# Kernel optimization log

Measured on AMD Instinct MI355X. Metric: run time of the kernel, lower is better.

Reference implementation:

```python
import jax, jax.numpy as jnp
import numpy as np

FIR = (1.0, 3.0, 3.0, 1.0)
FACTOR = 2
GAIN = 1.0


def _fir_kernel_2d():
    # _setup_kernel: 1D -> outer product, normalize, then scale by gain*factor^2
    k = np.asarray(FIR, dtype=np.float32)
    k = np.outer(k, k)
    k /= k.sum()
    return k * (GAIN * FACTOR ** 2)  # [4, 4]


def setup_inputs() -> dict:
    key = jax.random.key(0)
    kx, kw = jax.random.split(key)
    x = jax.random.normal(kx, (4, 256, 64, 64), dtype=jnp.float32)
    # DDPM variance-scaling init ~ U(-sqrt(3*var), sqrt(3*var)); plain scaled normal is fine for a numeric baseline
    w = jax.random.normal(kw, (256, 256, 3, 3), dtype=jnp.float32) * 0.02  # [outC, inC, 3, 3]
    return {"x": x, "w": w}


def reference(x, w):
    # Fused upsample(+FIR) conv: torch does conv_transpose2d(x, flip(w).permute(in,out), stride=2)
    # which is exactly a correlation of the stride-2 zero-dilated input with the ORIGINAL OIHW weight.
    N, C, H, W = x.shape
    outC, inC, kh, kw_ = w.shape
    h = jax.lax.conv_general_dilated(
        x, w,
        window_strides=(1, 1),
        padding=((kh - 1, kh - 1), (kw_ - 1, kw_ - 1)),
        lhs_dilation=(FACTOR, FACTOR),
        dimension_numbers=("NCHW", "OIHW", "NCHW"),
    )  # [N, outC, 2H+1, 2W+1]

    k = jnp.asarray(_fir_kernel_2d())  # [4,4]
    p = k.shape[0] - FACTOR - (kw_ - 1)          # = 0
    pad0 = (p + 1) // 2 + FACTOR - 1             # = 1
    pad1 = p // 2 + 1                            # = 1
    # upfirdn2d with up=1, down=1, pad=(pad0,pad1): pad then TRUE convolution (flipped kernel),
    # applied depthwise per channel.
    kflip = k[::-1, ::-1]
    kern = jnp.tile(kflip[None, None, :, :], (outC, 1, 1, 1))  # [outC, 1, 4, 4]
    out = jax.lax.conv_general_dilated(
        h, kern,
        window_strides=(1, 1),
        padding=((pad0, pad1), (pad0, pad1)),
        dimension_numbers=("NCHW", "OIHW", "NCHW"),
        feature_group_count=outC,
    )  # [N, outC, 2H, 2W]
    return out
```

## Files before the change

### kernel.cpp

```cpp
#include <hip/hip_runtime.h>
#include <hip/hip_bf16.h>


typedef short short2v __attribute__((ext_vector_type(2)));
typedef short bf16x8 __attribute__((ext_vector_type(8)));
typedef short short4v __attribute__((ext_vector_type(4)));
typedef float f32x2v __attribute__((ext_vector_type(2)));
typedef float f32x16 __attribute__((ext_vector_type(16)));
typedef float f32x4v __attribute__((ext_vector_type(4)));

static __device__ __forceinline__ short f2bf(float f) {
  __hip_bfloat16 h = __float2bfloat16(f);
  union { __hip_bfloat16 h; short s; } u; u.h = h;
  return u.s;
}
static __device__ __forceinline__ float bf2f(short s) {
  union { unsigned u; float f; } v; v.u = ((unsigned)(unsigned short)s) << 16;
  return v.f;
}

#define AS_SZ 18432
#define XS_BASE 36864
#define XS_SZ 8640
#define XS_STRIDE 48

__global__ __launch_bounds__(512, 2)
void fir_up_v17(const float* __restrict__ x, const float* __restrict__ w,
                float* __restrict__ out) {
  __shared__ __align__(16) char smem[54144];

  const int bid = blockIdx.x;
  const int wg = (bid & 7) * 64 + (bid >> 3);
  const int octile = wg >> 7;
  const int n = (wg >> 5) & 3;
  const int sp = wg & 31;
  const int atile = sp >> 2;
  const int btile = sp & 3;
  const int A0 = atile * 8, B0 = btile * 16;

  const int tid = threadIdx.x;
  const int wid = tid >> 6;
  const int lane = tid & 63;
  const int l31 = lane & 31, q = lane >> 5;

  const int COLSt[4]  = {17, 18, 17, 18};
  const int CELLSt[4] = {153, 162, 170, 180};
  const int NKt[4]    = {4, 2, 2, 1};
  const int KQt[4][4] = {{0,2,6,8},{1,7,7,7},{3,5,5,5},{4,4,4,4}};
  const int DYt[4][4] = {{0,0,1,1},{0,1,1,1},{0,0,0,0},{0,0,0,0}};
  const int DXt[4][4] = {{0,1,0,1},{0,0,0,0},{0,1,1,1},{0,0,0,0}};
  const int SEG0P[8]   = {0,0,0,1,1,2,2,3};
  const int SEG0FGB[8] = {0,2,4,0,3,0,3,0};
  const int SEG0NFG[8] = {2,2,1,3,3,3,3,4};

  const int p0w = SEG0P[wid];
  const int nk0 = NKt[p0w];
  const int nfg0 = SEG0NFG[wid];
  int aoff0[4];
#pragma unroll
  for (int s = 0; s < 4; ++s)
    aoff0[s] = KQt[p0w][s] * 2048 + l31 * 32 + q * 16;
  int boff0[4][4], valid0[4], hbase0[4];
#pragma unroll
  for (int fg = 0; fg < 4; ++fg) {
    const int cellraw = (SEG0FGB[wid] + fg) * 32 + l31;
    const int valid = cellraw < CELLSt[p0w];
    const int cell = valid ? cellraw : 0;
    const int cols = COLSt[p0w];
    const int r = cell / cols;
    const int c = cell - r * cols;
    valid0[fg] = valid;
    hbase0[fg] = p0w * 6400 + r * 20 + c;
#pragma unroll
    for (int s = 0; s < 4; ++s) {
      const int bc = (r + DYt[p0w][s]) * 18 + (c + DXt[p0w][s]);
      boff0[fg][s] = bc * XS_STRIDE + q * 16;
    }
  }
  const int aoff1 = 4 * 2048 + l31 * 32 + q * 16;
  int boff1[2], valid1[2], hbase1[2];
#pragma unroll
  for (int j = 0; j < 2; ++j) {
    const int cellraw = (4 + j) * 32 + l31;
    const int valid = cellraw < 180;
    const int cell = valid ? cellraw : 0;
    const int r = cell / 18;
    const int c = cell - r * 18;
    valid1[j] = valid;
    hbase1[j] = 3 * 6400 + r * 20 + c;
    boff1[j] = cell * XS_STRIDE + q * 16;
  }

  f32x16 acc[4][2];
#pragma unroll
  for (int fg = 0; fg < 4; ++fg)
#pragma unroll
    for (int mf = 0; mf < 2; ++mf)
#pragma unroll
      for (int e = 0; e < 16; ++e) acc[fg][mf][e] = 0.f;

  const int ocA = tid >> 3, icp = tid & 7;
  const float* wA = w + (size_t)(octile * 64 + ocA) * 2304 + icp * 18;
  int uic_[2], urow_[2], uf4g_[2], ugh_[2], ugw0_[2], uwb0_[2];
  bool uact_[2], urowok_[2], ual_[2], uint_[2];
#pragma unroll
  for (int t = 0; t < 2; ++t) {
    const int u = tid + t * 512;
    uact_[t] = u < 960;
    const int uu = uact_[t] ? u : 0;
    uic_[t] = uu / 60;
    const int rem = uu - uic_[t] * 60;
    urow_[t] = rem / 6;
    uf4g_[t] = rem - urow_[t] * 6;
    ugh_[t] = A0 - 1 + urow_[t];
    urowok_[t] = (ugh_[t] >= 0) & (ugh_[t] < 64);
    ugw0_[t] = B0 - 4 + 4 * uf4g_[t];
    ual_[t] = (ugw0_[t] >= 0) & (ugw0_[t] <= 60);
    uint_[t] = (uf4g_[t] >= 1) & (uf4g_[t] <= 4);
    uwb0_[t] = (urow_[t] * 18 + (4 * uf4g_[t] - 3)) * XS_STRIDE + uic_[t] * 2;
  }

  {
    char* xsw = smem + XS_BASE;
#pragma unroll
    for (int t = 0; t < 2; ++t) {
      if (uact_[t]) {
        float v[4] = {0.f, 0.f, 0.f, 0.f};
        if (urowok_[t]) {
          const float* base = x + (((size_t)(n * 256 + uic_[t])) * 64 + ugh_[t]) * 64;
          if (ual_[t]) {
            const f32x4v fv = *(const f32x4v*)(base + ugw0_[t]);
#pragma unroll
            for (int e = 0; e < 4; ++e) v[e] = fv[e];
          } else {
#pragma unroll
            for (int e = 0; e < 4; ++e) {
              const int gw = ugw0_[t] + e;
              v[e] = (gw >= 0 && gw < 64) ? base[gw] : 0.f;
            }
          }
        }
        if (uint_[t]) {
#pragma unroll
          for (int e = 0; e < 4; ++e)
            *(short*)(xsw + uwb0_[t] + e * XS_STRIDE) = f2bf(v[e]);
        } else {
#pragma unroll
          for (int e = 0; e < 4; ++e) {
            const int ww = 4 * uf4g_[t] + e - 3;
            if (ww >= 0 && ww < 18)
              *(short*)(xsw + (urow_[t] * 18 + ww) * XS_STRIDE + uic_[t] * 2) = f2bf(v[e]);
          }
        }
      }
    }
    float f18[18];
#pragma unroll
    for (int j = 0; j < 9; ++j)
      *(f32x2v*)&f18[2 * j] = *(const f32x2v*)(wA + 2 * j);
#pragma unroll
    for (int kq = 0; kq < 9; ++kq) {
      short2v pk;
      pk[0] = f2bf(f18[kq]);
      pk[1] = f2bf(f18[kq + 9]);
      *(short2v*)(smem + kq * 2048 + ocA * 32 + icp * 4) = pk;
    }
  }
  __syncthreads();

  for (int cc = 0; cc < 16; ++cc) {
    char* Asr = smem + (cc & 1) * AS_SZ;
    char* xsr = smem + XS_BASE + (cc & 1) * XS_SZ;
    char* Asw = smem + ((cc + 1) & 1) * AS_SZ;
    char* xsw = smem + XS_BASE + ((cc + 1) & 1) * XS_SZ;
    const bool have = cc < 15;

    float xv[2][4];
#pragma unroll
    for (int t = 0; t < 2; ++t) {
#pragma unroll
      for (int e = 0; e < 4; ++e) xv[t][e] = 0.f;
      if (have && uact_[t] && urowok_[t]) {
        const float* base =
            x + (((size_t)(n * 256 + (cc + 1) * 16 + uic_[t])) * 64 + ugh_[t]) * 64;
        if (ual_[t]) {
          const f32x4v fv = *(const f32x4v*)(base + ugw0_[t]);
#pragma unroll
          for (int e = 0; e < 4; ++e) xv[t][e] = fv[e];
        } else {
#pragma unroll
          for (int e = 0; e < 4; ++e) {
            const int gw = ugw0_[t] + e;
            xv[t][e] = (gw >= 0 && gw < 64) ? base[gw] : 0.f;
          }
        }
      }
    }

    __builtin_amdgcn_s_setprio(1);
#pragma unroll
    for (int s = 0; s < 4; ++s) {
      if (s < nk0) {
        const bf16x8 Aa = *(const bf16x8*)(Asr + aoff0[s]);
        const bf16x8 Ab = *(const bf16x8*)(Asr + aoff0[s] + 1024);
#pragma unroll
        for (int fg = 0; fg < 4; ++fg) {
          if (fg < nfg0) {
            const bf16x8 B = *(const bf16x8*)(xsr + boff0[fg][s]);
            acc[fg][0] = __builtin_amdgcn_mfma_f32_32x32x16_bf16(Aa, B, acc[fg][0], 0, 0, 0);
            acc[fg][1] = __builtin_amdgcn_mfma_f32_32x32x16_bf16(Ab, B, acc[fg][1], 0, 0, 0);
          }
        }
      }
    }
    if (wid == 2) {
      const bf16x8 Aa = *(const bf16x8*)(Asr + aoff1);
      const bf16x8 Ab = *(const bf16x8*)(Asr + aoff1 + 1024);
#pragma unroll
      for (int j = 0; j < 2; ++j) {
        const bf16x8 B = *(const bf16x8*)(xsr + boff1[j]);
        acc[1 + j][0] = __builtin_amdgcn_mfma_f32_32x32x16_bf16(Aa, B, acc[1 + j][0], 0, 0, 0);
        acc[1 + j][1] = __builtin_amdgcn_mfma_f32_32x32x16_bf16(Ab, B, acc[1 + j][1], 0, 0, 0);
      }
    }
    __builtin_amdgcn_s_setprio(0);

    if (have) {
#pragma unroll
      for (int t = 0; t < 2; ++t) {
        if (uact_[t]) {
          if (uint_[t]) {
#pragma unroll
            for (int e = 0; e < 4; ++e)
              *(short*)(xsw + uwb0_[t] + e * XS_STRIDE) = f2bf(xv[t][e]);
          } else {
#pragma unroll
            for (int e = 0; e < 4; ++e) {
              const int ww = 4 * uf4g_[t] + e - 3;
              if (ww >= 0 && ww < 18)
                *(short*)(xsw + (urow_[t] * 18 + ww) * XS_STRIDE + uic_[t] * 2) = f2bf(xv[t][e]);
            }
          }
        }
      }
      float f18[18];
      const float* wp = wA + (cc + 1) * 144;
#pragma unroll
      for (int j = 0; j < 9; ++j)
        *(f32x2v*)&f18[2 * j] = *(const f32x2v*)(wp + 2 * j);
#pragma unroll
      for (int kq = 0; kq < 9; ++kq) {
        short2v pk;
        pk[0] = f2bf(f18[kq]);
        pk[1] = f2bf(f18[kq + 9]);
        *(short2v*)(Asw + kq * 2048 + ocA * 32 + icp * 4) = pk;
      }
    }
    __syncthreads();
  }

  short* hl = (short*)smem;
  const float kf4[4] = {0.25f, 0.75f, 0.75f, 0.25f};
#pragma unroll
  for (int mf = 0; mf < 2; ++mf) {
    if (mf) __syncthreads();
#pragma unroll
    for (int fg = 0; fg < 4; ++fg) {
      if (fg < nfg0 && valid0[fg]) {
#pragma unroll
        for (int e = 0; e < 16; ++e) {
          const int ocl = (e & 3) + 8 * (e >> 2) + 4 * q;
          hl[hbase0[fg] + ocl * 200] = f2bf(acc[fg][mf][e]);
        }
      }
    }
    if (wid == 2) {
#pragma unroll
      for (int j = 0; j < 2; ++j) {
        if (valid1[j]) {
#pragma unroll
          for (int e = 0; e < 16; ++e) {
            const int ocl = (e & 3) + 8 * (e >> 2) + 4 * q;
            hl[hbase1[j] + ocl * 200] = f2bf(acc[1 + j][mf][e]);
          }
        }
      }
    }
    __syncthreads();
#pragma unroll
    for (int k = 0; k < 4; ++k) {
      const int v = tid + k * 512;
      const int g = v & 3;
      const int Yl = (v >> 2) & 15;
      const int ocl = v >> 6;
      float o[8];
#pragma unroll
      for (int xx = 0; xx < 8; ++xx) o[xx] = 0.f;
#pragma unroll
      for (int du = 0; du < 4; ++du) {
        const int ttp = Yl - 1 + du;
        const int py = ttp & 1;
        const int r = py ? ((Yl + du) >> 1) : (ttp >> 1);
        const int baseE = (py * 2) * 6400 + ocl * 200 + r * 20 + 4 * g;
        const int baseO = (py * 2 + 1) * 6400 + ocl * 200 + r * 20 + 4 * g;
        const short4v e0 = *(const short4v*)(hl + baseE);
        const short4v e1 = *(const short4v*)(hl + baseE + 4);
        const short4v o0 = *(const short4v*)(hl + baseO);
        const short4v o1 = *(const short4v*)(hl + baseO + 4);
        float E[8], O[8];
#pragma unroll
        for (int i = 0; i < 4; ++i) {
          E[i] = bf2f(e0[i]); E[i + 4] = bf2f(e1[i]);
          O[i] = bf2f(o0[i]); O[i + 4] = bf2f(o1[i]);
        }
        float rx[8];
        rx[0] = 0.25f*O[0] + 0.75f*E[0] + 0.75f*O[1] + 0.25f*E[1];
        rx[1] = 0.25f*E[0] + 0.75f*O[1] + 0.75f*E[1] + 0.25f*O[2];
        rx[2] = 0.25f*O[1] + 0.75f*E[1] + 0.75f*O[2] + 0.25f*E[2];
        rx[3] = 0.25f*E[1] + 0.75f*O[2] + 0.75f*E[2] + 0.25f*O[3];
        rx[4] = 0.25f*O[2] + 0.75f*E[2] + 0.75f*O[3] + 0.25f*E[3];
        rx[5] = 0.25f*E[2] + 0.75f*O[3] + 0.75f*E[3] + 0.25f*O[4];
        rx[6] = 0.25f*O[3] + 0.75f*E[3] + 0.75f*O[4] + 0.25f*E[4];
        rx[7] = 0.25f*E[3] + 0.75f*O[4] + 0.75f*E[4] + 0.25f*O[5];
        const float ky = kf4[du];
#pragma unroll
        for (int xx = 0; xx < 8; ++xx) o[xx] += ky * rx[xx];
      }
      const int oc = octile * 64 + mf * 32 + ocl;
      const int Y = atile * 16 + Yl;
      const int X0 = btile * 32 + g * 8;
      float* op = out + (((size_t)(n * 256 + oc)) * 128 + Y) * 128 + X0;
      f32x4v v0, v1;
      v0[0] = o[0]; v0[1] = o[1]; v0[2] = o[2]; v0[3] = o[3];
      v1[0] = o[4]; v1[1] = o[5]; v1[2] = o[6]; v1[3] = o[7];
      *(f32x4v*)op = v0;
      *(f32x4v*)(op + 4) = v1;
    }
  }
}

extern "C" void kernel_launch(void* const* d_in, const int* in_sizes, int n_in,
                              void* d_out, int out_size, void* d_ws, size_t ws_size,
                              hipStream_t stream) {
  (void)in_sizes; (void)n_in; (void)out_size; (void)d_ws; (void)ws_size;
  const float* x = (const float*)d_in[0];
  const float* w = (const float*)d_in[1];
  float* out = (float*)d_out;
  hipLaunchKernelGGL(fir_up_v17, dim3(512), dim3(512), 0, stream, x, w, out);
}
```

Baseline: 85.31 us.

## Double input-channel chunk per stage and rebalance phase-3 MFMA work across waves

Each pipeline stage now stages 32 input channels instead of 16, so the main loop runs 8 iterations with half as many barriers. Each stage issues two K=16 MFMA halves per A/B fragment. The next stage's weight loads are moved ahead of the MFMA block so their latency overlaps compute. One phase-3 fragment group moves from wave 7 to wave 0 to even out MFMA counts. The cost is that LDS per block grows to about 118 KB, which likely leaves room for only one 512-thread block per CU despite the launch bound of 2, and the larger staging also raises register pressure.

```diff
diff --git a/kernel.cpp b/kernel.cpp
--- a/kernel.cpp
+++ b/kernel.cpp
@@ -2,10 +2,9 @@
 #include <hip/hip_bf16.h>
 
 
-typedef short short2v __attribute__((ext_vector_type(2)));
+typedef short bf16x4v __attribute__((ext_vector_type(4)));
 typedef short bf16x8 __attribute__((ext_vector_type(8)));
 typedef short short4v __attribute__((ext_vector_type(4)));
-typedef float f32x2v __attribute__((ext_vector_type(2)));
 typedef float f32x16 __attribute__((ext_vector_type(16)));
 typedef float f32x4v __attribute__((ext_vector_type(4)));
 
@@ -19,15 +18,17 @@
   return v.f;
 }
 
-#define AS_SZ 18432
-#define XS_BASE 36864
-#define XS_SZ 8640
-#define XS_STRIDE 48
+#define AS_SZ 46080
+#define KQ_PLANE 5120
+#define AB_OFF 2560
+#define XS_BASE 92160
+#define XS_SZ 14400
+#define XS_STRIDE 80
 
 __global__ __launch_bounds__(512, 2)
-void fir_up_v17(const float* __restrict__ x, const float* __restrict__ w,
+void fir_up_v18(const float* __restrict__ x, const float* __restrict__ w,
                 float* __restrict__ out) {
-  __shared__ __align__(16) char smem[54144];
+  __shared__ __align__(16) char smem[120960];
 
   const int bid = blockIdx.x;
   const int wg = (bid & 7) * 64 + (bid >> 3);
@@ -51,7 +52,7 @@
   const int DXt[4][4] = {{0,1,0,1},{0,0,0,0},{0,1,1,1},{0,0,0,0}};
   const int SEG0P[8]   = {0,0,0,1,1,2,2,3};
   const int SEG0FGB[8] = {0,2,4,0,3,0,3,0};
-  const int SEG0NFG[8] = {2,2,1,3,3,3,3,4};
+  const int SEG0NFG[8] = {2,2,1,3,3,3,3,3};
 
   const int p0w = SEG0P[wid];
   const int nk0 = NKt[p0w];
@@ -59,10 +60,10 @@
   int aoff0[4];
 #pragma unroll
   for (int s = 0; s < 4; ++s)
-    aoff0[s] = KQt[p0w][s] * 2048 + l31 * 32 + q * 16;
-  int boff0[4][4], valid0[4], hbase0[4];
-#pragma unroll
-  for (int fg = 0; fg < 4; ++fg) {
+    aoff0[s] = KQt[p0w][s] * KQ_PLANE + l31 * 80 + q * 16;
+  int boff0[3][4], valid0[3], hbase0[3];
+#pragma unroll
+  for (int fg = 0; fg < 3; ++fg) {
     const int cellraw = (SEG0FGB[wid] + fg) * 32 + l31;
     const int valid = cellraw < CELLSt[p0w];
     const int cell = valid ? cellraw : 0;
@@ -77,36 +78,43 @@
       boff0[fg][s] = bc * XS_STRIDE + q * 16;
     }
   }
-  const int aoff1 = 4 * 2048 + l31 * 32 + q * 16;
+  const int aoff1 = 4 * KQ_PLANE + l31 * 80 + q * 16;
+  int boffW0, hbaseW0;
+  {
+    const int cell = 96 + l31;
+    const int r = cell / 18, c = cell - r * 18;
+    hbaseW0 = 3 * 6400 + r * 20 + c;
+    boffW0 = cell * XS_STRIDE + q * 16;
+  }
   int boff1[2], valid1[2], hbase1[2];
 #pragma unroll
   for (int j = 0; j < 2; ++j) {
     const int cellraw = (4 + j) * 32 + l31;
     const int valid = cellraw < 180;
     const int cell = valid ? cellraw : 0;
-    const int r = cell / 18;
-    const int c = cell - r * 18;
+    const int r = cell / 18, c = cell - r * 18;
     valid1[j] = valid;
     hbase1[j] = 3 * 6400 + r * 20 + c;
     boff1[j] = cell * XS_STRIDE + q * 16;
   }
 
-  f32x16 acc[4][2];
-#pragma unroll
-  for (int fg = 0; fg < 4; ++fg)
+  f32x16 acc[3][2];
+#pragma unroll
+  for (int fg = 0; fg < 3; ++fg)
 #pragma unroll
     for (int mf = 0; mf < 2; ++mf)
 #pragma unroll
       for (int e = 0; e < 16; ++e) acc[fg][mf][e] = 0.f;
 
-  const int ocA = tid >> 3, icp = tid & 7;
-  const float* wA = w + (size_t)(octile * 64 + ocA) * 2304 + icp * 18;
-  int uic_[2], urow_[2], uf4g_[2], ugh_[2], ugw0_[2], uwb0_[2];
-  bool uact_[2], urowok_[2], ual_[2], uint_[2];
-#pragma unroll
-  for (int t = 0; t < 2; ++t) {
+  const int ocA = tid >> 3, icq = tid & 7;
+  const float* wA = w + (size_t)(octile * 64 + ocA) * 2304 + icq * 36;
+  const int awb = ocA * 80 + icq * 8;
+  int uic_[4], urow_[4], uf4g_[4], ugh_[4], ugw0_[4], uwb0_[4];
+  bool uact_[4], urowok_[4], ual_[4], uint_[4];
+#pragma unroll
+  for (int t = 0; t < 4; ++t) {
     const int u = tid + t * 512;
-    uact_[t] = u < 960;
+    uact_[t] = u < 1920;
     const int uu = uact_[t] ? u : 0;
     uic_[t] = uu / 60;
     const int rem = uu - uic_[t] * 60;
@@ -123,7 +131,7 @@
   {
     char* xsw = smem + XS_BASE;
 #pragma unroll
-    for (int t = 0; t < 2; ++t) {
+    for (int t = 0; t < 4; ++t) {
       if (uact_[t]) {
         float v[4] = {0.f, 0.f, 0.f, 0.f};
         if (urowok_[t]) {
@@ -154,35 +162,35 @@
         }
       }
     }
-    float f18[18];
+    float f36[36];
 #pragma unroll
     for (int j = 0; j < 9; ++j)
-      *(f32x2v*)&f18[2 * j] = *(const f32x2v*)(wA + 2 * j);
+      *(f32x4v*)&f36[4 * j] = *(const f32x4v*)(wA + 4 * j);
 #pragma unroll
     for (int kq = 0; kq < 9; ++kq) {
-      short2v pk;
-      pk[0] = f2bf(f18[kq]);
-      pk[1] = f2bf(f18[kq + 9]);
-      *(short2v*)(smem + kq * 2048 + ocA * 32 + icp * 4) = pk;
+      bf16x4v pk;
+#pragma unroll
+      for (int v = 0; v < 4; ++v) pk[v] = f2bf(f36[v * 9 + kq]);
+      *(bf16x4v*)(smem + kq * KQ_PLANE + awb) = pk;
     }
   }
   __syncthreads();
 
-  for (int cc = 0; cc < 16; ++cc) {
+  for (int cc = 0; cc < 8; ++cc) {
     char* Asr = smem + (cc & 1) * AS_SZ;
     char* xsr = smem + XS_BASE + (cc & 1) * XS_SZ;
     char* Asw = smem + ((cc + 1) & 1) * AS_SZ;
     char* xsw = smem + XS_BASE + ((cc + 1) & 1) * XS_SZ;
-    const bool have = cc < 15;
-
-    float xv[2][4];
-#pragma unroll
-    for (int t = 0; t < 2; ++t) {
+    const bool have = cc < 7;
+
+    float xv[4][4];
+#pragma unroll
+    for (int t = 0; t < 4; ++t) {
 #pragma unroll
       for (int e = 0; e < 4; ++e) xv[t][e] = 0.f;
       if (have && uact_[t] && urowok_[t]) {
         const float* base =
-            x + (((size_t)(n * 256 + (cc + 1) * 16 + uic_[t])) * 64 + ugh_[t]) * 64;
+            x + (((size_t)(n * 256 + (cc + 1) * 32 + uic_[t])) * 64 + ugh_[t]) * 64;
         if (ual_[t]) {
           const f32x4v fv = *(const f32x4v*)(base + ugw0_[t]);
 #pragma unroll
@@ -196,38 +204,59 @@
         }
       }
     }
+    f32x4v wv[9];
+#pragma unroll
+    for (int j = 0; j < 9; ++j) {
+      if (have) wv[j] = *(const f32x4v*)(wA + (cc + 1) * 288 + 4 * j);
+    }
 
     __builtin_amdgcn_s_setprio(1);
 #pragma unroll
     for (int s = 0; s < 4; ++s) {
       if (s < nk0) {
-        const bf16x8 Aa = *(const bf16x8*)(Asr + aoff0[s]);
-        const bf16x8 Ab = *(const bf16x8*)(Asr + aoff0[s] + 1024);
-#pragma unroll
-        for (int fg = 0; fg < 4; ++fg) {
-          if (fg < nfg0) {
-            const bf16x8 B = *(const bf16x8*)(xsr + boff0[fg][s]);
-            acc[fg][0] = __builtin_amdgcn_mfma_f32_32x32x16_bf16(Aa, B, acc[fg][0], 0, 0, 0);
-            acc[fg][1] = __builtin_amdgcn_mfma_f32_32x32x16_bf16(Ab, B, acc[fg][1], 0, 0, 0);
-          }
-        }
+#pragma unroll
+        for (int h = 0; h < 2; ++h) {
+          const bf16x8 Aa = *(const bf16x8*)(Asr + aoff0[s] + h * 32);
+          const bf16x8 Ab = *(const bf16x8*)(Asr + aoff0[s] + h * 32 + AB_OFF);
+#pragma unroll
+          for (int fg = 0; fg < 3; ++fg) {
+            if (fg < nfg0) {
+              const bf16x8 B = *(const bf16x8*)(xsr + boff0[fg][s] + h * 32);
+              acc[fg][0] = __builtin_amdgcn_mfma_f32_32x32x16_bf16(Aa, B, acc[fg][0], 0, 0, 0);
+              acc[fg][1] = __builtin_amdgcn_mfma_f32_32x32x16_bf16(Ab, B, acc[fg][1], 0, 0, 0);
+            }
+          }
+        }
+      }
+    }
+    if (wid == 0) {
+#pragma unroll
+      for (int h = 0; h < 2; ++h) {
+        const bf16x8 Aa = *(const bf16x8*)(Asr + aoff1 + h * 32);
+        const bf16x8 Ab = *(const bf16x8*)(Asr + aoff1 + h * 32 + AB_OFF);
+        const bf16x8 B = *(const bf16x8*)(xsr + boffW0 + h * 32);
+        acc[2][0] = __builtin_amdgcn_mfma_f32_32x32x16_bf16(Aa, B, acc[2][0], 0, 0, 0);
+        acc[2][1] = __builtin_amdgcn_mfma_f32_32x32x16_bf16(Ab, B, acc[2][1], 0, 0, 0);
       }
     }
     if (wid == 2) {
-      const bf16x8 Aa = *(const bf16x8*)(Asr + aoff1);
-      const bf16x8 Ab = *(const bf16x8*)(Asr + aoff1 + 1024);
-#pragma unroll
-      for (int j = 0; j < 2; ++j) {
-        const bf16x8 B = *(const bf16x8*)(xsr + boff1[j]);
-        acc[1 + j][0] = __builtin_amdgcn_mfma_f32_32x32x16_bf16(Aa, B, acc[1 + j][0], 0, 0, 0);
-        acc[1 + j][1] = __builtin_amdgcn_mfma_f32_32x32x16_bf16(Ab, B, acc[1 + j][1], 0, 0, 0);
+#pragma unroll
+      for (int h = 0; h < 2; ++h) {
+        const bf16x8 Aa = *(const bf16x8*)(Asr + aoff1 + h * 32);
+        const bf16x8 Ab = *(const bf16x8*)(Asr + aoff1 + h * 32 + AB_OFF);
+#pragma unroll
+        for (int j = 0; j < 2; ++j) {
+          const bf16x8 B = *(const bf16x8*)(xsr + boff1[j] + h * 32);
+          acc[1 + j][0] = __builtin_amdgcn_mfma_f32_32x32x16_bf16(Aa, B, acc[1 + j][0], 0, 0, 0);
+          acc[1 + j][1] = __builtin_amdgcn_mfma_f32_32x32x16_bf16(Ab, B, acc[1 + j][1], 0, 0, 0);
+        }
       }
     }
     __builtin_amdgcn_s_setprio(0);
 
     if (have) {
 #pragma unroll
-      for (int t = 0; t < 2; ++t) {
+      for (int t = 0; t < 4; ++t) {
         if (uact_[t]) {
           if (uint_[t]) {
 #pragma unroll
@@ -243,17 +272,19 @@
           }
         }
       }
-      float f18[18];
-      const float* wp = wA + (cc + 1) * 144;
-#pragma unroll
-      for (int j = 0; j < 9; ++j)
-        *(f32x2v*)&f18[2 * j] = *(const f32x2v*)(wp + 2 * j);
 #pragma unroll
       for (int kq = 0; kq < 9; ++kq) {
-        short2v pk;
-        pk[0] = f2bf(f18[kq]);
-        pk[1] = f2bf(f18[kq + 9]);
-        *(short2v*)(Asw + kq * 2048 + ocA * 32 + icp * 4) = pk;
+        bf16x4v pk;
+#pragma unroll
+        for (int v = 0; v < 4; ++v) pk[v] = f2bf(wv[v & 1 ? (v == 1 ? 2 : 6) : (v == 0 ? 0 : 4)][0]);
+        (void)pk;
+        bf16x4v pk2;
+#pragma unroll
+        for (int v = 0; v < 4; ++v) {
+          const int flat = v * 9 + kq;
+          pk2[v] = f2bf(wv[flat >> 2][flat & 3]);
+        }
+        *(bf16x4v*)(Asw + kq * KQ_PLANE + awb) = pk2;
       }
     }
     __syncthreads();
@@ -265,13 +296,20 @@
   for (int mf = 0; mf < 2; ++mf) {
     if (mf) __syncthreads();
 #pragma unroll
-    for (int fg = 0; fg < 4; ++fg) {
+    for (int fg = 0; fg < 3; ++fg) {
       if (fg < nfg0 && valid0[fg]) {
 #pragma unroll
         for (int e = 0; e < 16; ++e) {
           const int ocl = (e & 3) + 8 * (e >> 2) + 4 * q;
           hl[hbase0[fg] + ocl * 200] = f2bf(acc[fg][mf][e]);
         }
+      }
+    }
+    if (wid == 0) {
+#pragma unroll
+      for (int e = 0; e < 16; ++e) {
+        const int ocl = (e & 3) + 8 * (e >> 2) + 4 * q;
+        hl[hbaseW0 + ocl * 200] = f2bf(acc[2][mf][e]);
       }
     }
     if (wid == 2) {
@@ -346,5 +384,5 @@
   const float* x = (const float*)d_in[0];
   const float* w = (const float*)d_in[1];
   float* out = (float*)d_out;
-  hipLaunchKernelGGL(fir_up_v17, dim3(512), dim3(512), 0, stream, x, w, out);
+  hipLaunchKernelGGL(fir_up_v18, dim3(512), dim3(512), 0, stream, x, w, out);
 }
```

Measured after the change: 81.59 us. -4.4%, faster.
